# Optimization experiments

Hardware: AMD Instinct MI355X
Metric: run time of the kernel (lower is better)

Reference implementation:

```python
import jax, jax.numpy as jnp
import numpy as np

THRESHOLD = 0.1
EPS = 1e-06


def _bilinear_warp(img, flow):
    """Backward-warp img [B,1,H,W] by flow [B,2,H,W] with bilinear sampling,
    zero padding for out-of-range taps (F.grid_sample zeros-padding semantics)."""
    B, _, H, W = img.shape
    imgf = img[:, 0].reshape(B, H * W)                      # [B, H*W]
    ys, xs = jnp.meshgrid(jnp.arange(H, dtype=flow.dtype),
                          jnp.arange(W, dtype=flow.dtype), indexing='ij')
    x = xs[None] + flow[:, 0]                               # [B,H,W] sample x
    y = ys[None] + flow[:, 1]                               # [B,H,W] sample y
    x0 = jnp.floor(x)
    y0 = jnp.floor(y)
    wx = x - x0
    wy = y - y0
    x0i = x0.astype(jnp.int32)
    y0i = y0.astype(jnp.int32)

    def tap(xi, yi):
        inb = ((xi >= 0) & (xi < W) & (yi >= 0) & (yi < H)).astype(img.dtype)
        idx = (jnp.clip(yi, 0, H - 1) * W + jnp.clip(xi, 0, W - 1)).reshape(B, H * W)
        vals = jnp.take_along_axis(imgf, idx, axis=1).reshape(B, H, W)
        return vals * inb

    out = (tap(x0i, y0i) * (1 - wx) * (1 - wy)
           + tap(x0i + 1, y0i) * wx * (1 - wy)
           + tap(x0i, y0i + 1) * (1 - wx) * wy
           + tap(x0i + 1, y0i + 1) * wx * wy)
    return out[:, None]                                     # [B,1,H,W]


def _forward(img1, img2, flow, event_voxels, valid_mask):
    B, _, H, W = flow.shape
    C = event_voxels.shape[1]
    rgb_w = jnp.array([0.299, 0.587, 0.114], dtype=img1.dtype)
    gray1 = jnp.einsum('bchw,c->bhw', img1, rgb_w)[:, None]  # [B,1,H,W]
    gray2 = jnp.einsum('bchw,c->bhw', img2, rgb_w)[:, None]
    warped_gray2 = _bilinear_warp(gray2, flow)
    normalized_change = jnp.tanh((warped_gray2 - gray1) * 5.0)[:, 0]  # [B,H,W]
    pos = jax.nn.relu(normalized_change)
    neg = jax.nn.relu(-normalized_change)

    # pred_events: ch0=pos, ch1=neg, ch i+2 = pos*w + neg*(1-w), w=(i+1)/(C-1)
    rem = C - 2
    w = jnp.arange(1, rem + 1, dtype=pos.dtype) / (rem + 1)          # [rem]
    mix = pos[:, None] * w[None, :, None, None] + neg[:, None] * (1 - w)[None, :, None, None]
    pred_events = jnp.concatenate([pos[:, None], neg[:, None], mix], axis=1)  # [B,C,H,W]

    flow_mag = jnp.sqrt(flow[:, 0] ** 2 + flow[:, 1] ** 2)
    event_mask = (flow_mag > THRESHOLD).astype(flow.dtype)[:, None]  # [B,1,H,W]
    combined_mask = valid_mask * event_mask                          # broadcasts over C
    combined_mask = jnp.broadcast_to(combined_mask, pred_events.shape)

    mask_sum = combined_mask.sum() + EPS
    pred_m = pred_events * combined_mask
    gt_m = event_voxels * combined_mask
    l1_loss = jnp.abs(pred_m - gt_m).sum() / mask_sum

    # batched correlation over (b,c)
    pred_flat = pred_m.reshape(B, C, -1)
    gt_flat = gt_m.reshape(B, C, -1)
    pn = pred_flat - pred_flat.mean(axis=-1, keepdims=True)
    gn = gt_flat - gt_flat.mean(axis=-1, keepdims=True)
    num = (pn * gn).sum(axis=-1)                                     # [B,C]
    den = jnp.linalg.norm(pn, axis=-1) * jnp.linalg.norm(gn, axis=-1) + EPS
    corr = num / den
    valid = combined_mask.sum(axis=(2, 3)) > 0                        # [B,C]
    corr_loss = jnp.where(valid, 1.0 - corr, 0.0).sum() / (B * C)

    loss = l1_loss + 0.5 * corr_loss
    return loss, pred_events


def setup_inputs() -> dict:
    key = jax.random.key(0)
    k1, k2, k3, k4, k5 = jax.random.split(key, 5)
    B, H, W, C = 8, 480, 640, 5
    return {
        'img1': jax.random.uniform(k1, (B, 3, H, W), dtype=jnp.float32),
        'img2': jax.random.uniform(k2, (B, 3, H, W), dtype=jnp.float32),
        'flow': jax.random.normal(k3, (B, 2, H, W), dtype=jnp.float32),
        'event_voxels': jax.random.normal(k4, (B, C, H, W), dtype=jnp.float32),
        'valid_mask': jax.random.uniform(k5, (B, 1, H, W), dtype=jnp.float32),
    }


def reference(img1, img2, flow, event_voxels, valid_mask):
    return _forward(img1, img2, flow, event_voxels, valid_mask)
```

## Files before the change

kernel.cpp:

```cpp
#include <hip/hip_runtime.h>
#include <math.h>

#define BB 8
#define HH 480
#define WW 640
#define CC 5
#define HW (HH * WW)
#define NBLK 300

#define PARTIAL_OFFSET 4096
#define GRAY2_OFFSET (PARTIAL_OFFSET + 2400 * 32 * 4)

__device__ __forceinline__ float fast_tanh5(float d) {
    float ez = __expf(-10.0f * d);
    return (1.0f - ez) * __builtin_amdgcn_rcpf(1.0f + ez);
}

__device__ __forceinline__ float mixc(int c, float pos, float neg) {
    if (c == 0) return pos;
    if (c == 1) return neg;
    const float w = 0.25f * (float)(c - 1);
    return w * pos + (1.0f - w) * neg;
}

__device__ __forceinline__ float wave_sum_dpp(float v) {
    v += __int_as_float(__builtin_amdgcn_update_dpp(0, __float_as_int(v), 0x111, 0xf, 0xf, false));
    v += __int_as_float(__builtin_amdgcn_update_dpp(0, __float_as_int(v), 0x112, 0xf, 0xf, false));
    v += __int_as_float(__builtin_amdgcn_update_dpp(0, __float_as_int(v), 0x114, 0xf, 0xf, false));
    v += __int_as_float(__builtin_amdgcn_update_dpp(0, __float_as_int(v), 0x118, 0xf, 0xf, false));
    v += __int_as_float(__builtin_amdgcn_update_dpp(0, __float_as_int(v), 0x142, 0xa, 0xf, false));
    v += __int_as_float(__builtin_amdgcn_update_dpp(0, __float_as_int(v), 0x143, 0xc, 0xf, false));
    return v;
}

__global__ __launch_bounds__(256) void k_gray2(const float* __restrict__ img2,
                                               float* __restrict__ gray2) {
    int gid = blockIdx.x * blockDim.x + threadIdx.x;
    int idx4 = gid * 4;
    if (idx4 >= BB * HW) return;
    int b = idx4 / HW;
    int p = idx4 - b * HW;
    const float* base = img2 + (size_t)b * 3 * HW + p;
    float4 r = *(const float4*)(base);
    float4 g = *(const float4*)(base + HW);
    float4 bl = *(const float4*)(base + 2 * HW);
    float4 o;
    o.x = 0.299f * r.x + 0.587f * g.x + 0.114f * bl.x;
    o.y = 0.299f * r.y + 0.587f * g.y + 0.114f * bl.y;
    o.z = 0.299f * r.z + 0.587f * g.z + 0.114f * bl.z;
    o.w = 0.299f * r.w + 0.587f * g.w + 0.114f * bl.w;
    *(float4*)(gray2 + idx4) = o;
}

__global__ __launch_bounds__(256, 2) void k_main(
    const float* __restrict__ img1, const float* __restrict__ flow,
    const float* __restrict__ ev, const float* __restrict__ vmask,
    const float* __restrict__ gray2, float* __restrict__ pred_out,
    float* __restrict__ partial)
{
    const int b = blockIdx.y;
    const float* i1  = img1  + (size_t)b * 3 * HW;
    const float* fl  = flow  + (size_t)b * 2 * HW;
    const float* evb = ev    + (size_t)b * CC * HW;
    const float* vm  = vmask + (size_t)b * HW;
    const float* g2  = gray2 + (size_t)b * HW;
    float* po = pred_out + (size_t)b * CC * HW;

    const int tid = threadIdx.x;
    const int P   = blockIdx.x * 1024;
    const int p4  = P + 4 * tid;
    const int py  = p4 / WW;
    const int px0 = p4 - py * WW;

    __shared__ float sdata[4][27];

    float4 fx4 = *(const float4*)(fl + p4);
    float4 fy4 = *(const float4*)(fl + HW + p4);

    float fxa[4] = { fx4.x, fx4.y, fx4.z, fx4.w };
    float fya[4] = { fy4.x, fy4.y, fy4.z, fy4.w };

    int   adr[4][4];
    float wgt[4][4];
#pragma unroll
    for (int j = 0; j < 4; ++j) {
        float fx = fxa[j], fy = fya[j];
        float x = (float)(px0 + j) + fx;
        float y = (float)py + fy;
        float x0f = floorf(x);
        float y0f = floorf(y);
        float wx = x - x0f;
        float wy = y - y0f;
        int x0 = (int)x0f, y0 = (int)y0f;
        int x1 = x0 + 1,   y1 = y0 + 1;
        int cx0 = min(max(x0, 0), WW - 1);
        int cx1 = min(max(x1, 0), WW - 1);
        int cy0 = min(max(y0, 0), HH - 1);
        int cy1 = min(max(y1, 0), HH - 1);
        float ix0 = (x0 >= 0 && x0 < WW) ? 1.0f : 0.0f;
        float ix1 = (x1 >= 0 && x1 < WW) ? 1.0f : 0.0f;
        float iy0 = (y0 >= 0 && y0 < HH) ? 1.0f : 0.0f;
        float iy1 = (y1 >= 0 && y1 < HH) ? 1.0f : 0.0f;
        adr[j][0] = cy0 * WW + cx0;
        adr[j][1] = cy0 * WW + cx1;
        adr[j][2] = cy1 * WW + cx0;
        adr[j][3] = cy1 * WW + cx1;
        wgt[j][0] = (1.0f - wx) * (1.0f - wy) * ix0 * iy0;
        wgt[j][1] = wx * (1.0f - wy) * ix1 * iy0;
        wgt[j][2] = (1.0f - wx) * wy * ix0 * iy1;
        wgt[j][3] = wx * wy * ix1 * iy1;
    }

    float tv[4][4];
#pragma unroll
    for (int j = 0; j < 4; ++j)
#pragma unroll
        for (int t = 0; t < 4; ++t) tv[j][t] = g2[adr[j][t]];

    float4 c0 = *(const float4*)(i1 + p4);
    float4 c1 = *(const float4*)(i1 + HW + p4);
    float4 c2 = *(const float4*)(i1 + 2 * HW + p4);
    float4 vm4 = *(const float4*)(vm + p4);
    float4 ev4[CC];
#pragma unroll
    for (int c = 0; c < CC; ++c) ev4[c] = *(const float4*)(evb + c * HW + p4);

    float g1a[4] = {
        0.299f * c0.x + 0.587f * c1.x + 0.114f * c2.x,
        0.299f * c0.y + 0.587f * c1.y + 0.114f * c2.y,
        0.299f * c0.z + 0.587f * c1.z + 0.114f * c2.z,
        0.299f * c0.w + 0.587f * c1.w + 0.114f * c2.w };
    float vma[4] = { vm4.x, vm4.y, vm4.z, vm4.w };

    float acc[27];
#pragma unroll
    for (int i = 0; i < 27; ++i) acc[i] = 0.0f;

    float posA[4], negA[4];

#pragma unroll
    for (int j = 0; j < 4; ++j) {
        float warp = tv[j][0] * wgt[j][0] + tv[j][1] * wgt[j][1]
                   + tv[j][2] * wgt[j][2] + tv[j][3] * wgt[j][3];

        float nc  = fast_tanh5(warp - g1a[j]);
        float pos = fmaxf(nc, 0.0f);
        float neg = fmaxf(-nc, 0.0f);
        posA[j] = pos;
        negA[j] = neg;

        float fx = fxa[j], fy = fya[j];
        float m = ((fx * fx + fy * fy) > 0.01f) ? vma[j] : 0.0f;
        acc[1] += m;

        const float ga[CC] = { ev4[0][j], ev4[1][j], ev4[2][j], ev4[3][j], ev4[4][j] };
#pragma unroll
        for (int c = 0; c < CC; ++c) {
            float pm = mixc(c, pos, neg) * m;
            float gm = ga[c] * m;
            acc[0] += fabsf(pm - gm);
            acc[2 + c * 5 + 0] += pm;
            acc[2 + c * 5 + 1] += gm;
            acc[2 + c * 5 + 2] += pm * gm;
            acc[2 + c * 5 + 3] += pm * pm;
            acc[2 + c * 5 + 4] += gm * gm;
        }
    }

    const int lane = tid & 63;
    float npos[3], nneg[3];
#pragma unroll
    for (int j = 0; j < 3; ++j) {
        npos[j] = __shfl_down(posA[j], 1, 64);
        nneg[j] = __shfl_down(negA[j], 1, 64);
    }

#pragma unroll
    for (int c = 0; c < CC; ++c) {
        float* ob = po + c * HW + P + 4 * tid;
        if (lane < 63) {
            float4 v;
            v.x = mixc(c, posA[3], negA[3]);
            v.y = mixc(c, npos[0], nneg[0]);
            v.z = mixc(c, npos[1], nneg[1]);
            v.w = mixc(c, npos[2], nneg[2]);
            *(float4*)(ob + 3) = v;
        } else {
            ob[3] = mixc(c, posA[3], negA[3]);
        }
        if (lane == 0) {
            ob[0] = mixc(c, posA[0], negA[0]);
            ob[1] = mixc(c, posA[1], negA[1]);
            ob[2] = mixc(c, posA[2], negA[2]);
        }
    }

    const int wid = tid >> 6;
#pragma unroll
    for (int i = 0; i < 27; ++i) acc[i] = wave_sum_dpp(acc[i]);
    if (lane == 63) {
#pragma unroll
        for (int i = 0; i < 27; ++i) sdata[wid][i] = acc[i];
    }

    __syncthreads();

    if (tid < 27) {
        float s = sdata[0][tid] + sdata[1][tid] + sdata[2][tid] + sdata[3][tid];
        partial[(size_t)(b * NBLK + blockIdx.x) * 32 + tid] = s;
    }
}

__global__ void k_reduce(const float* __restrict__ partial, double* __restrict__ stats) {
    int bi = blockIdx.x;
    int b = bi / 27;
    int i = bi - b * 27;
    int t = threadIdx.x;
    double s = 0.0;
    for (int k = t; k < NBLK; k += 64)
        s += (double)partial[(size_t)(b * NBLK + k) * 32 + i];
    for (int off = 32; off > 0; off >>= 1) s += __shfl_down(s, off, 64);
    if (t == 0) {
        if (i == 0)      stats[210 + b] = s;
        else if (i == 1) stats[1 + b] = s;
        else             stats[9 + b * 25 + (i - 2)] = s;
    }
}

__global__ void k_final(const double* __restrict__ stats, float* __restrict__ out) {
    int t = threadIdx.x;
    double contrib = 0.0;
    if (t < BB * CC) {
        int b = t / CC;
        int c = t - b * CC;
        const double* s = stats + 9 + b * 25 + c * 5;
        double Sp = s[0], Sg = s[1], Spg = s[2], Spp = s[3], Sgg = s[4];
        const double N = (double)HW;
        double num  = Spg - Sp * Sg / N;
        double varp = Spp - Sp * Sp / N; if (varp < 0.0) varp = 0.0;
        double varg = Sgg - Sg * Sg / N; if (varg < 0.0) varg = 0.0;
        double den  = sqrt(varp) * sqrt(varg) + 1e-6;
        double corr = num / den;
        bool valid = stats[1 + b] > 0.0;
        contrib = valid ? (1.0 - corr) : 0.0;
    }
    for (int off = 32; off > 0; off >>= 1) contrib += __shfl_down(contrib, off, 64);
    if (t == 0) {
        double msum_total = 0.0, l1sum = 0.0;
        for (int b = 0; b < BB; ++b) { msum_total += stats[1 + b]; l1sum += stats[210 + b]; }
        double mask_sum = (double)CC * msum_total + 1e-6;
        double l1_loss = l1sum / mask_sum;
        double corr_loss = contrib / (double)(BB * CC);
        out[0] = (float)(l1_loss + 0.5 * corr_loss);
    }
}

extern "C" void kernel_launch(void* const* d_in, const int* in_sizes, int n_in,
                              void* d_out, int out_size, void* d_ws, size_t ws_size,
                              hipStream_t stream) {
    const float* img1  = (const float*)d_in[0];
    const float* img2  = (const float*)d_in[1];
    const float* flow  = (const float*)d_in[2];
    const float* ev    = (const float*)d_in[3];
    const float* vmask = (const float*)d_in[4];
    float* out = (float*)d_out;

    double* stats   = (double*)d_ws;
    float*  partial = (float*)((char*)d_ws + PARTIAL_OFFSET);
    float*  gray2   = (float*)((char*)d_ws + GRAY2_OFFSET);

    int ngroups = BB * HW / 4;
    k_gray2<<<(ngroups + 255) / 256, 256, 0, stream>>>(img2, gray2);

    dim3 grid(NBLK, BB);
    k_main<<<grid, 256, 0, stream>>>(img1, flow, ev, vmask, gray2, out + 1, partial);

    k_reduce<<<BB * 27, 64, 0, stream>>>(partial, stats);

    k_final<<<1, 64, 0, stream>>>(stats, out);
}
```

Before: 50.15 us.

## Fuse gray conversion into warp gather and compress per-channel statistics

New measurement: 67.88 us. 35.4% more time.

```diff
diff --git a/kernel.cpp b/kernel.cpp
--- a/kernel.cpp
+++ b/kernel.cpp
@@ -7,9 +7,9 @@
 #define CC 5
 #define HW (HH * WW)
 #define NBLK 300
+#define NST 21
 
 #define PARTIAL_OFFSET 4096
-#define GRAY2_OFFSET (PARTIAL_OFFSET + 2400 * 32 * 4)
 
 __device__ __forceinline__ float fast_tanh5(float d) {
     float ez = __expf(-10.0f * d);
@@ -33,37 +33,18 @@
     return v;
 }
 
-__global__ __launch_bounds__(256) void k_gray2(const float* __restrict__ img2,
-                                               float* __restrict__ gray2) {
-    int gid = blockIdx.x * blockDim.x + threadIdx.x;
-    int idx4 = gid * 4;
-    if (idx4 >= BB * HW) return;
-    int b = idx4 / HW;
-    int p = idx4 - b * HW;
-    const float* base = img2 + (size_t)b * 3 * HW + p;
-    float4 r = *(const float4*)(base);
-    float4 g = *(const float4*)(base + HW);
-    float4 bl = *(const float4*)(base + 2 * HW);
-    float4 o;
-    o.x = 0.299f * r.x + 0.587f * g.x + 0.114f * bl.x;
-    o.y = 0.299f * r.y + 0.587f * g.y + 0.114f * bl.y;
-    o.z = 0.299f * r.z + 0.587f * g.z + 0.114f * bl.z;
-    o.w = 0.299f * r.w + 0.587f * g.w + 0.114f * bl.w;
-    *(float4*)(gray2 + idx4) = o;
-}
-
 __global__ __launch_bounds__(256, 2) void k_main(
-    const float* __restrict__ img1, const float* __restrict__ flow,
-    const float* __restrict__ ev, const float* __restrict__ vmask,
-    const float* __restrict__ gray2, float* __restrict__ pred_out,
+    const float* __restrict__ img1, const float* __restrict__ img2,
+    const float* __restrict__ flow, const float* __restrict__ ev,
+    const float* __restrict__ vmask, float* __restrict__ pred_out,
     float* __restrict__ partial)
 {
     const int b = blockIdx.y;
     const float* i1  = img1  + (size_t)b * 3 * HW;
+    const float* i2  = img2  + (size_t)b * 3 * HW;
     const float* fl  = flow  + (size_t)b * 2 * HW;
     const float* evb = ev    + (size_t)b * CC * HW;
     const float* vm  = vmask + (size_t)b * HW;
-    const float* g2  = gray2 + (size_t)b * HW;
     float* po = pred_out + (size_t)b * CC * HW;
 
     const int tid = threadIdx.x;
@@ -72,16 +53,23 @@
     const int py  = p4 / WW;
     const int px0 = p4 - py * WW;
 
-    __shared__ float sdata[4][27];
+    __shared__ float sdata[4][NST];
 
     float4 fx4 = *(const float4*)(fl + p4);
     float4 fy4 = *(const float4*)(fl + HW + p4);
+    float4 c0  = *(const float4*)(i1 + p4);
+    float4 c1  = *(const float4*)(i1 + HW + p4);
+    float4 c2  = *(const float4*)(i1 + 2 * HW + p4);
+    float4 vm4 = *(const float4*)(vm + p4);
+    float4 ev4[CC];
+#pragma unroll
+    for (int c = 0; c < CC; ++c) ev4[c] = *(const float4*)(evb + c * HW + p4);
 
     float fxa[4] = { fx4.x, fx4.y, fx4.z, fx4.w };
     float fya[4] = { fy4.x, fy4.y, fy4.z, fy4.w };
 
-    int   adr[4][4];
-    float wgt[4][4];
+    int   adr[16];
+    float wgt[16];
 #pragma unroll
     for (int j = 0; j < 4; ++j) {
         float fx = fxa[j], fy = fya[j];
@@ -97,33 +85,29 @@
         int cx1 = min(max(x1, 0), WW - 1);
         int cy0 = min(max(y0, 0), HH - 1);
         int cy1 = min(max(y1, 0), HH - 1);
-        float ix0 = (x0 >= 0 && x0 < WW) ? 1.0f : 0.0f;
-        float ix1 = (x1 >= 0 && x1 < WW) ? 1.0f : 0.0f;
-        float iy0 = (y0 >= 0 && y0 < HH) ? 1.0f : 0.0f;
-        float iy1 = (y1 >= 0 && y1 < HH) ? 1.0f : 0.0f;
-        adr[j][0] = cy0 * WW + cx0;
-        adr[j][1] = cy0 * WW + cx1;
-        adr[j][2] = cy1 * WW + cx0;
-        adr[j][3] = cy1 * WW + cx1;
-        wgt[j][0] = (1.0f - wx) * (1.0f - wy) * ix0 * iy0;
-        wgt[j][1] = wx * (1.0f - wy) * ix1 * iy0;
-        wgt[j][2] = (1.0f - wx) * wy * ix0 * iy1;
-        wgt[j][3] = wx * wy * ix1 * iy1;
-    }
-
-    float tv[4][4];
-#pragma unroll
-    for (int j = 0; j < 4; ++j)
-#pragma unroll
-        for (int t = 0; t < 4; ++t) tv[j][t] = g2[adr[j][t]];
-
-    float4 c0 = *(const float4*)(i1 + p4);
-    float4 c1 = *(const float4*)(i1 + HW + p4);
-    float4 c2 = *(const float4*)(i1 + 2 * HW + p4);
-    float4 vm4 = *(const float4*)(vm + p4);
-    float4 ev4[CC];
-#pragma unroll
-    for (int c = 0; c < CC; ++c) ev4[c] = *(const float4*)(evb + c * HW + p4);
+        float wx0 = (1.0f - wx) * ((x0 >= 0 && x0 < WW) ? 1.0f : 0.0f);
+        float wx1 = wx          * ((x1 >= 0 && x1 < WW) ? 1.0f : 0.0f);
+        float wy0 = (1.0f - wy) * ((y0 >= 0 && y0 < HH) ? 1.0f : 0.0f);
+        float wy1 = wy          * ((y1 >= 0 && y1 < HH) ? 1.0f : 0.0f);
+        adr[j * 4 + 0] = cy0 * WW + cx0;
+        adr[j * 4 + 1] = cy0 * WW + cx1;
+        adr[j * 4 + 2] = cy1 * WW + cx0;
+        adr[j * 4 + 3] = cy1 * WW + cx1;
+        wgt[j * 4 + 0] = wx0 * wy0;
+        wgt[j * 4 + 1] = wx1 * wy0;
+        wgt[j * 4 + 2] = wx0 * wy1;
+        wgt[j * 4 + 3] = wx1 * wy1;
+    }
+
+    float tap[16];
+#pragma unroll
+    for (int t = 0; t < 16; ++t) {
+        int o = adr[t];
+        float r  = i2[o];
+        float g  = i2[o + HW];
+        float bl = i2[o + 2 * HW];
+        tap[t] = 0.299f * r + 0.587f * g + 0.114f * bl;
+    }
 
     float g1a[4] = {
         0.299f * c0.x + 0.587f * c1.x + 0.114f * c2.x,
@@ -132,16 +116,16 @@
         0.299f * c0.w + 0.587f * c1.w + 0.114f * c2.w };
     float vma[4] = { vm4.x, vm4.y, vm4.z, vm4.w };
 
-    float acc[27];
-#pragma unroll
-    for (int i = 0; i < 27; ++i) acc[i] = 0.0f;
+    float acc[NST];
+#pragma unroll
+    for (int i = 0; i < NST; ++i) acc[i] = 0.0f;
 
     float posA[4], negA[4];
 
 #pragma unroll
     for (int j = 0; j < 4; ++j) {
-        float warp = tv[j][0] * wgt[j][0] + tv[j][1] * wgt[j][1]
-                   + tv[j][2] * wgt[j][2] + tv[j][3] * wgt[j][3];
+        float warp = tap[j*4+0] * wgt[j*4+0] + tap[j*4+1] * wgt[j*4+1]
+                   + tap[j*4+2] * wgt[j*4+2] + tap[j*4+3] * wgt[j*4+3];
 
         float nc  = fast_tanh5(warp - g1a[j]);
         float pos = fmaxf(nc, 0.0f);
@@ -151,19 +135,24 @@
 
         float fx = fxa[j], fy = fya[j];
         float m = ((fx * fx + fy * fy) > 0.01f) ? vma[j] : 0.0f;
+
+        float posm = pos * m;
+        float negm = neg * m;
         acc[1] += m;
+        acc[2] += posm;
+        acc[3] += negm;
+        acc[4] += posm * posm;
+        acc[5] += negm * negm;
 
         const float ga[CC] = { ev4[0][j], ev4[1][j], ev4[2][j], ev4[3][j], ev4[4][j] };
 #pragma unroll
         for (int c = 0; c < CC; ++c) {
-            float pm = mixc(c, pos, neg) * m;
+            float pm = mixc(c, posm, negm);
             float gm = ga[c] * m;
-            acc[0] += fabsf(pm - gm);
-            acc[2 + c * 5 + 0] += pm;
-            acc[2 + c * 5 + 1] += gm;
-            acc[2 + c * 5 + 2] += pm * gm;
-            acc[2 + c * 5 + 3] += pm * pm;
-            acc[2 + c * 5 + 4] += gm * gm;
+            acc[0]      += fabsf(pm - gm);
+            acc[6 + c]  += gm;
+            acc[11 + c] += gm * gm;
+            acc[16 + c] += pm * gm;
         }
     }
 
@@ -197,15 +186,15 @@
 
     const int wid = tid >> 6;
 #pragma unroll
-    for (int i = 0; i < 27; ++i) acc[i] = wave_sum_dpp(acc[i]);
+    for (int i = 0; i < NST; ++i) acc[i] = wave_sum_dpp(acc[i]);
     if (lane == 63) {
 #pragma unroll
-        for (int i = 0; i < 27; ++i) sdata[wid][i] = acc[i];
+        for (int i = 0; i < NST; ++i) sdata[wid][i] = acc[i];
     }
 
     __syncthreads();
 
-    if (tid < 27) {
+    if (tid < NST) {
         float s = sdata[0][tid] + sdata[1][tid] + sdata[2][tid] + sdata[3][tid];
         partial[(size_t)(b * NBLK + blockIdx.x) * 32 + tid] = s;
     }
@@ -213,18 +202,14 @@
 
 __global__ void k_reduce(const float* __restrict__ partial, double* __restrict__ stats) {
     int bi = blockIdx.x;
-    int b = bi / 27;
-    int i = bi - b * 27;
+    int b = bi / NST;
+    int i = bi - b * NST;
     int t = threadIdx.x;
     double s = 0.0;
     for (int k = t; k < NBLK; k += 64)
         s += (double)partial[(size_t)(b * NBLK + k) * 32 + i];
     for (int off = 32; off > 0; off >>= 1) s += __shfl_down(s, off, 64);
-    if (t == 0) {
-        if (i == 0)      stats[210 + b] = s;
-        else if (i == 1) stats[1 + b] = s;
-        else             stats[9 + b * 25 + (i - 2)] = s;
-    }
+    if (t == 0) stats[b * NST + i] = s;
 }
 
 __global__ void k_final(const double* __restrict__ stats, float* __restrict__ out) {
@@ -233,21 +218,31 @@
     if (t < BB * CC) {
         int b = t / CC;
         int c = t - b * CC;
-        const double* s = stats + 9 + b * 25 + c * 5;
-        double Sp = s[0], Sg = s[1], Spg = s[2], Spp = s[3], Sgg = s[4];
+        const double* s = stats + b * NST;
+        const double wA[CC] = { 1.0, 0.0, 0.25, 0.50, 0.75 };
+        const double wB[CC] = { 0.0, 1.0, 0.75, 0.50, 0.25 };
+        double a = wA[c], bb = wB[c];
+        double Sp  = a * s[2] + bb * s[3];
+        double Spp = a * a * s[4] + bb * bb * s[5];
+        double Sg  = s[6 + c];
+        double Sgg = s[11 + c];
+        double Spg = s[16 + c];
         const double N = (double)HW;
         double num  = Spg - Sp * Sg / N;
         double varp = Spp - Sp * Sp / N; if (varp < 0.0) varp = 0.0;
         double varg = Sgg - Sg * Sg / N; if (varg < 0.0) varg = 0.0;
         double den  = sqrt(varp) * sqrt(varg) + 1e-6;
         double corr = num / den;
-        bool valid = stats[1 + b] > 0.0;
+        bool valid = s[1] > 0.0;
         contrib = valid ? (1.0 - corr) : 0.0;
     }
     for (int off = 32; off > 0; off >>= 1) contrib += __shfl_down(contrib, off, 64);
     if (t == 0) {
         double msum_total = 0.0, l1sum = 0.0;
-        for (int b = 0; b < BB; ++b) { msum_total += stats[1 + b]; l1sum += stats[210 + b]; }
+        for (int b = 0; b < BB; ++b) {
+            msum_total += stats[b * NST + 1];
+            l1sum      += stats[b * NST + 0];
+        }
         double mask_sum = (double)CC * msum_total + 1e-6;
         double l1_loss = l1sum / mask_sum;
         double corr_loss = contrib / (double)(BB * CC);
@@ -267,15 +262,11 @@
 
     double* stats   = (double*)d_ws;
     float*  partial = (float*)((char*)d_ws + PARTIAL_OFFSET);
-    float*  gray2   = (float*)((char*)d_ws + GRAY2_OFFSET);
-
-    int ngroups = BB * HW / 4;
-    k_gray2<<<(ngroups + 255) / 256, 256, 0, stream>>>(img2, gray2);
 
     dim3 grid(NBLK, BB);
-    k_main<<<grid, 256, 0, stream>>>(img1, flow, ev, vmask, gray2, out + 1, partial);
-
-    k_reduce<<<BB * 27, 64, 0, stream>>>(partial, stats);
+    k_main<<<grid, 256, 0, stream>>>(img1, img2, flow, ev, vmask, out + 1, partial);
+
+    k_reduce<<<BB * NST, 64, 0, stream>>>(partial, stats);
 
     k_final<<<1, 64, 0, stream>>>(stats, out);
 }
```
